# Performance work log

Hardware: AMD Instinct MI355X
Metric: run time of the kernel (lower is better)

Reference implementation:

```python
import jax, jax.numpy as jnp
import numpy as np

H = 64        # gru_hiddens
HEADS = 4     # n_heads
HID = 64      # n_hidden (is_concat=False -> out_features)
RT = 4        # role_types
APT = 3       # agents per type
N_AMB = 1023  # ambiguous agents; N = 1 + N_AMB = 1024
SLOPE = 0.2


def _leaky(x):
    return jnp.where(x >= 0, x, SLOPE * x)


def _linear(x, W, b):
    return x @ W.T + b


def setup_inputs() -> dict:
    key = jax.random.key(0)
    ks = jax.random.split(key, 18)
    s = 0.1
    return {
        "hidden": jax.random.normal(ks[0], (1, H), jnp.float32),
        "ambiguous": jax.random.normal(ks[1], (N_AMB, H), jnp.float32),
        "type_agents": jax.random.normal(ks[2], (RT, APT, 1, H), jnp.float32),
        # per-role-type routing MLPs and merge/self MLPs
        "W_self": jax.random.normal(ks[3], (H, H), jnp.float32) * s,
        "b_self": jnp.zeros((H,), jnp.float32),
        "W_merge": jax.random.normal(ks[4], (H, 2 * H), jnp.float32) * s,
        "b_merge": jnp.zeros((H,), jnp.float32),
        "W_trans": jax.random.normal(ks[5], (RT, H, H), jnp.float32) * s,
        "b_trans": jnp.zeros((RT, H), jnp.float32),
        # GATv2 params (no biases)
        "W_l": jax.random.normal(ks[6], (HEADS * HID, H), jnp.float32) * s,
        "W_r": jax.random.normal(ks[7], (HEADS * HID, H), jnp.float32) * s,
        "w_attn": jax.random.normal(ks[8], (HID,), jnp.float32) * s,
        # type_define MLP: 2H -> 64 -> 128 -> RT
        "Wd0": jax.random.normal(ks[9], (64, 2 * H), jnp.float32) * s,
        "bd0": jnp.zeros((64,), jnp.float32),
        "Wd1": jax.random.normal(ks[10], (128, 64), jnp.float32) * s,
        "bd1": jnp.zeros((128,), jnp.float32),
        "Wd2": jax.random.normal(ks[11], (RT, 128), jnp.float32) * s,
        "bd2": jnp.zeros((RT,), jnp.float32),
    }


def reference(hidden, ambiguous, type_agents,
              W_self, b_self, W_merge, b_merge, W_trans, b_trans,
              W_l, W_r, w_attn,
              Wd0, bd0, Wd1, bd1, Wd2, bd2):
    # per-role-type routing + merge
    hidden_1 = _linear(hidden, W_self, b_self)  # [1, H]
    for t in range(RT):
        # mean over agents of trans_mlp[t](agent)
        tmp = (jnp.einsum('aih,oh->aio', type_agents[t], W_trans[t]) + b_trans[t]).mean(axis=0)
        hidden_1 = _leaky(_linear(jnp.concatenate([hidden_1, tmp], axis=-1), W_merge, b_merge))

    h = jnp.concatenate([hidden_1, ambiguous], axis=0)  # [N, H], N = 1 + N_AMB
    n = h.shape[0]

    # GATv2 dense pairwise attention (adjacency all-True; dropout in eval = identity)
    g_l = (h @ W_l.T).reshape(n, HEADS, HID)
    g_r = (h @ W_r.T).reshape(n, HEADS, HID)
    # g_sum[i, j] = g_l[j] + g_r[i]  -> [N, N, HEADS, HID]
    g_sum = g_l[None, :, :, :] + g_r[:, None, :, :]
    e = jnp.einsum('ijhf,f->ijh', _leaky(g_sum), w_attn)  # [N, N, HEADS]
    a = jax.nn.softmax(e, axis=1)
    attn_res = jnp.einsum('ijh,jhf->ihf', a, g_r)  # [N, HEADS, HID]
    gat_out = attn_res.mean(axis=1)  # is_concat=False -> mean over heads, [N, HID]

    hidden_2 = gat_out[0]  # [HID]
    rep = jnp.broadcast_to(hidden_2[None, :], (ambiguous.shape[0], HID))
    x = jnp.concatenate([ambiguous, rep], axis=-1)  # [N_AMB, 2H]
    x = _leaky(_linear(x, Wd0, bd0))
    x = _leaky(_linear(x, Wd1, bd1))
    x = _linear(x, Wd2, bd2)
    return jax.nn.sigmoid(x)  # [N_AMB, RT]
```

## Files before the change

### kernel.cpp

```cpp
#include <hip/hip_runtime.h>
#include <math.h>

#define SLOPE 0.2f
#define KA_BLK 128
#define KA_ROWS 8
#define PART_STRIDE 320

__device__ __forceinline__ float leaky(float x) { return x >= 0.f ? x : SLOPE * x; }


__global__ __launch_bounds__(256) void kA_gat(
    const float* __restrict__ hidden, const float* __restrict__ ambiguous,
    const float* __restrict__ type_agents,
    const float* __restrict__ W_self, const float* __restrict__ b_self,
    const float* __restrict__ W_merge, const float* __restrict__ b_merge,
    const float* __restrict__ W_trans, const float* __restrict__ b_trans,
    const float* __restrict__ W_l, const float* __restrict__ W_r,
    const float* __restrict__ w_attn, float* __restrict__ ws)
{
    __shared__ __align__(16) float sh[128];
    __shared__ __align__(16) float tm[64];
    __shared__ __align__(16) float h1[64];
    __shared__ __align__(16) float hrow[KA_ROWS][64];

    const int t = threadIdx.x;
    const int o = t & 63;
    const int r = t >> 6;
    const int b = blockIdx.x;

    float4 wr[16];
    {
        const float4* Wr4 = (const float4*)(W_r + t * 64);
#pragma unroll
        for (int k = 0; k < 16; k++) wr[k] = Wr4[k];
    }

    if (r != 0) {
        int u = t - 64;
#pragma unroll
        for (int i = 0; i < 3; i++) {
            int idx = u + 192 * i;
            if (idx < KA_ROWS * 64) {
                int rl = idx >> 6, c = idx & 63;
                int j = b * KA_ROWS + rl;
                hrow[rl][c] = (j == 0) ? 0.f : ambiguous[(j - 1) * 64 + c];
            }
        }
    } else {
        float hv;
        {
            float acc = b_self[o];
            const float4* w4 = (const float4*)(W_self + o * 64);
#pragma unroll
            for (int k = 0; k < 16; k++) {
                float4 w = w4[k];
                acc += w.x * hidden[k*4+0] + w.y * hidden[k*4+1]
                     + w.z * hidden[k*4+2] + w.w * hidden[k*4+3];
            }
            hv = acc;
        }
        for (int tt = 0; tt < 4; tt++) {
            sh[o] = hv;
            tm[o] = (type_agents[tt*192 + o] + type_agents[tt*192 + 64 + o]
                   + type_agents[tt*192 + 128 + o]) * (1.f / 3.f);
            __threadfence_block();
            float tv = b_trans[tt*64 + o];
            {
                const float4* w4 = (const float4*)(W_trans + tt*4096 + o*64);
#pragma unroll
                for (int k = 0; k < 16; k++) {
                    float4 w = w4[k];
                    tv += w.x * tm[k*4+0] + w.y * tm[k*4+1]
                        + w.z * tm[k*4+2] + w.w * tm[k*4+3];
                }
            }
            sh[64 + o] = tv;
            __threadfence_block();
            float acc = b_merge[o];
            const float4* w4 = (const float4*)(W_merge + o * 128);
#pragma unroll
            for (int k = 0; k < 32; k++) {
                float4 w = w4[k];
                acc += w.x * sh[k*4+0] + w.y * sh[k*4+1]
                     + w.z * sh[k*4+2] + w.w * sh[k*4+3];
            }
            hv = leaky(acc);
            __threadfence_block();
        }
        h1[o] = hv;
    }
    __syncthreads();
    if (b == 0 && t < 64) hrow[0][o] = h1[o];

    float g0 = 0.f;
#pragma unroll
    for (int k = 0; k < 16; k++) {
        float4 w = wr[k];
        g0 += w.x * h1[k*4+0] + w.y * h1[k*4+1] + w.z * h1[k*4+2] + w.w * h1[k*4+3];
    }
    __syncthreads();

    float accl[KA_ROWS], accr[KA_ROWS];
#pragma unroll
    for (int rr = 0; rr < KA_ROWS; rr++) { accl[rr] = 0.f; accr[rr] = 0.f; }
    {
        const float4* Wl4 = (const float4*)(W_l + t * 64);
#pragma unroll
        for (int kk = 0; kk < 16; kk++) {
            float4 a = Wl4[kk];
            float4 c = wr[kk];
#pragma unroll
            for (int rr = 0; rr < KA_ROWS; rr++) {
                float x0 = hrow[rr][kk*4+0], x1 = hrow[rr][kk*4+1];
                float x2 = hrow[rr][kk*4+2], x3 = hrow[rr][kk*4+3];
                accl[rr] += a.x*x0 + a.y*x1 + a.z*x2 + a.w*x3;
                accr[rr] += c.x*x0 + c.y*x1 + c.z*x2 + c.w*x3;
            }
        }
    }

    const float wa = w_attn[o];
    float numsum = 0.f, denp = 0.f;
#pragma unroll
    for (int rr = 0; rr < KA_ROWS; rr++) {
        float ec = leaky(accl[rr] + g0) * wa;
#pragma unroll
        for (int off = 32; off; off >>= 1) ec += __shfl_xor(ec, off, 64);
        float w = expf(ec);
        numsum += w * accr[rr];
        denp   += w;
    }
    ws[b * PART_STRIDE + t] = numsum;
    if (o == 0) ws[b * PART_STRIDE + 256 + r] = denp;
}

__global__ __launch_bounds__(256) void kB_mlp(
    const float* __restrict__ ambiguous,
    const float* __restrict__ Wd0, const float* __restrict__ bd0,
    const float* __restrict__ Wd1, const float* __restrict__ bd1,
    const float* __restrict__ Wd2, const float* __restrict__ bd2,
    const float* __restrict__ ws, float* __restrict__ out)
{
    __shared__ __align__(16) float x[4][128];
    __shared__ __align__(16) float y0[4][64];
    __shared__ __align__(16) float y1[4][128];
    __shared__ __align__(16) float hs[4][64];
    const int t  = threadIdx.x;
    const int o  = t & 63;
    const int r  = t >> 6;
    const int r0 = blockIdx.x * 4;

    {
        int row = r0 + r;
        x[r][o] = (row < 1023) ? ambiguous[row * 64 + o] : 0.f;
    }

    float nsum = 0.f;
#pragma unroll 16
    for (int bb = 0; bb < KA_BLK; bb++) nsum += ws[bb * PART_STRIDE + t];

    float d = ws[o * PART_STRIDE + 256 + r]
            + ws[(o + 64) * PART_STRIDE + 256 + r];
#pragma unroll
    for (int off = 32; off; off >>= 1) d += __shfl_xor(d, off, 64);
    hs[r][o] = nsum / d;
    __syncthreads();
    if (t < 64) {
        float h2 = 0.25f * (hs[0][o] + hs[1][o] + hs[2][o] + hs[3][o]);
        x[0][64 + o] = h2; x[1][64 + o] = h2; x[2][64 + o] = h2; x[3][64 + o] = h2;
    }
    __syncthreads();

    {
        float acc = bd0[o];
        const float4* w4 = (const float4*)(Wd0 + o * 128);
        const float4* xr = (const float4*)(&x[r][0]);
#pragma unroll
        for (int kk = 0; kk < 32; kk++) {
            float4 w = w4[kk]; float4 xv = xr[kk];
            acc += w.x*xv.x + w.y*xv.y + w.z*xv.z + w.w*xv.w;
        }
        y0[r][o] = leaky(acc);
    }
    __syncthreads();

#pragma unroll
    for (int rep = 0; rep < 2; rep++) {
        int idx = rep * 256 + t;
        int rr = idx >> 7, oo = idx & 127;
        float acc = bd1[oo];
        const float4* w4 = (const float4*)(Wd1 + oo * 64);
        const float4* yr = (const float4*)(&y0[rr][0]);
#pragma unroll
        for (int kk = 0; kk < 16; kk++) {
            float4 w = w4[kk]; float4 yv = yr[kk];
            acc += w.x*yv.x + w.y*yv.y + w.z*yv.z + w.w*yv.w;
        }
        y1[rr][oo] = leaky(acc);
    }
    __syncthreads();

    if (t < 16) {
        int rr = t >> 2, c = t & 3;
        int row = r0 + rr;
        if (row < 1023) {
            float acc = bd2[c];
            const float4* w4 = (const float4*)(Wd2 + c * 128);
            const float4* yr = (const float4*)(&y1[rr][0]);
#pragma unroll
            for (int kk = 0; kk < 32; kk++) {
                float4 w = w4[kk]; float4 yv = yr[kk];
                acc += w.x*yv.x + w.y*yv.y + w.z*yv.z + w.w*yv.w;
            }
            out[row * 4 + c] = 1.f / (1.f + expf(-acc));
        }
    }
}

extern "C" void kernel_launch(void* const* d_in, const int* in_sizes, int n_in,
                              void* d_out, int out_size, void* d_ws, size_t ws_size,
                              hipStream_t stream)
{
    const float* hidden      = (const float*)d_in[0];
    const float* ambiguous   = (const float*)d_in[1];
    const float* type_agents = (const float*)d_in[2];
    const float* W_self      = (const float*)d_in[3];
    const float* b_self      = (const float*)d_in[4];
    const float* W_merge     = (const float*)d_in[5];
    const float* b_merge     = (const float*)d_in[6];
    const float* W_trans     = (const float*)d_in[7];
    const float* b_trans     = (const float*)d_in[8];
    const float* W_l         = (const float*)d_in[9];
    const float* W_r         = (const float*)d_in[10];
    const float* w_attn      = (const float*)d_in[11];
    const float* Wd0         = (const float*)d_in[12];
    const float* bd0         = (const float*)d_in[13];
    const float* Wd1         = (const float*)d_in[14];
    const float* bd1         = (const float*)d_in[15];
    const float* Wd2         = (const float*)d_in[16];
    const float* bd2         = (const float*)d_in[17];
    float* ws  = (float*)d_ws;
    float* out = (float*)d_out;

    kA_gat<<<KA_BLK, 256, 0, stream>>>(hidden, ambiguous, type_agents,
                                       W_self, b_self, W_merge, b_merge,
                                       W_trans, b_trans, W_l, W_r, w_attn, ws);
    kB_mlp<<<256, 256, 0, stream>>>(ambiguous, Wd0, bd0, Wd1, bd1, Wd2, bd2, ws, out);
}
```

Measured before the change: 129.1 us.

## Parallelize role-type transforms across warps and double GAT block count

The four per-role-type trans-MLP products are now computed in parallel by the four wavefronts before the serial merge chain, which shortens the critical path that only wavefront 0 ran before. W_l is preloaded into registers alongside W_r. The GAT kernel now launches 256 blocks of 4 rows instead of 128 blocks of 8, for more parallelism, and the MLP kernel sums twice as many partial sums and denominators. The cost is higher register pressure from holding both weight matrices and more redundant per-block work on the hidden-state chain.

```diff
diff --git a/kernel.cpp b/kernel.cpp
--- a/kernel.cpp
+++ b/kernel.cpp
@@ -2,8 +2,8 @@
 #include <math.h>
 
 #define SLOPE 0.2f
-#define KA_BLK 128
-#define KA_ROWS 8
+#define KA_BLK 256
+#define KA_ROWS 4
 #define PART_STRIDE 320
 
 __device__ __forceinline__ float leaky(float x) { return x >= 0.f ? x : SLOPE * x; }
@@ -18,8 +18,9 @@
     const float* __restrict__ W_l, const float* __restrict__ W_r,
     const float* __restrict__ w_attn, float* __restrict__ ws)
 {
-    __shared__ __align__(16) float sh[128];
-    __shared__ __align__(16) float tm[64];
+    __shared__ __align__(16) float tmean[4][64];
+    __shared__ __align__(16) float tmpv[4][64];
+    __shared__ __align__(16) float hstage[64];
     __shared__ __align__(16) float h1[64];
     __shared__ __align__(16) float hrow[KA_ROWS][64];
 
@@ -28,17 +29,46 @@
     const int r = t >> 6;
     const int b = blockIdx.x;
 
-    float4 wr[16];
+    float4 wr[16], wl[16];
     {
         const float4* Wr4 = (const float4*)(W_r + t * 64);
-#pragma unroll
-        for (int k = 0; k < 16; k++) wr[k] = Wr4[k];
+        const float4* Wl4 = (const float4*)(W_l + t * 64);
+#pragma unroll
+        for (int k = 0; k < 16; k++) { wr[k] = Wr4[k]; wl[k] = Wl4[k]; }
+    }
+
+    float hv = 0.f;
+    if (r == 0) {
+        float acc = b_self[o];
+        const float4* w4 = (const float4*)(W_self + o * 64);
+#pragma unroll
+        for (int k = 0; k < 16; k++) {
+            float4 w = w4[k];
+            acc += w.x * hidden[k*4+0] + w.y * hidden[k*4+1]
+                 + w.z * hidden[k*4+2] + w.w * hidden[k*4+3];
+        }
+        hv = acc;
+    }
+
+    tmean[r][o] = (type_agents[r*192 + o] + type_agents[r*192 + 64 + o]
+                 + type_agents[r*192 + 128 + o]) * (1.f / 3.f);
+    __threadfence_block();
+    {
+        float tv = b_trans[r*64 + o];
+        const float4* w4 = (const float4*)(W_trans + r*4096 + o*64);
+        const float4* tm4 = (const float4*)(&tmean[r][0]);
+#pragma unroll
+        for (int k = 0; k < 16; k++) {
+            float4 w = w4[k]; float4 m = tm4[k];
+            tv += w.x*m.x + w.y*m.y + w.z*m.z + w.w*m.w;
+        }
+        tmpv[r][o] = tv;
     }
 
     if (r != 0) {
         int u = t - 64;
 #pragma unroll
-        for (int i = 0; i < 3; i++) {
+        for (int i = 0; i < 2; i++) {
             int idx = u + 192 * i;
             if (idx < KA_ROWS * 64) {
                 int rl = idx >> 6, c = idx & 63;
@@ -46,43 +76,23 @@
                 hrow[rl][c] = (j == 0) ? 0.f : ambiguous[(j - 1) * 64 + c];
             }
         }
-    } else {
-        float hv;
-        {
-            float acc = b_self[o];
-            const float4* w4 = (const float4*)(W_self + o * 64);
-#pragma unroll
-            for (int k = 0; k < 16; k++) {
-                float4 w = w4[k];
-                acc += w.x * hidden[k*4+0] + w.y * hidden[k*4+1]
-                     + w.z * hidden[k*4+2] + w.w * hidden[k*4+3];
-            }
-            hv = acc;
-        }
+    }
+    __syncthreads();
+
+    if (r == 0) {
+        const float4* w4 = (const float4*)(W_merge + o * 128);
         for (int tt = 0; tt < 4; tt++) {
-            sh[o] = hv;
-            tm[o] = (type_agents[tt*192 + o] + type_agents[tt*192 + 64 + o]
-                   + type_agents[tt*192 + 128 + o]) * (1.f / 3.f);
-            __threadfence_block();
-            float tv = b_trans[tt*64 + o];
-            {
-                const float4* w4 = (const float4*)(W_trans + tt*4096 + o*64);
-#pragma unroll
-                for (int k = 0; k < 16; k++) {
-                    float4 w = w4[k];
-                    tv += w.x * tm[k*4+0] + w.y * tm[k*4+1]
-                        + w.z * tm[k*4+2] + w.w * tm[k*4+3];
-                }
-            }
-            sh[64 + o] = tv;
+            hstage[o] = hv;
             __threadfence_block();
             float acc = b_merge[o];
-            const float4* w4 = (const float4*)(W_merge + o * 128);
-#pragma unroll
-            for (int k = 0; k < 32; k++) {
-                float4 w = w4[k];
-                acc += w.x * sh[k*4+0] + w.y * sh[k*4+1]
-                     + w.z * sh[k*4+2] + w.w * sh[k*4+3];
+            const float4* hs4 = (const float4*)(&hstage[0]);
+            const float4* tp4 = (const float4*)(&tmpv[tt][0]);
+#pragma unroll
+            for (int k = 0; k < 16; k++) {
+                float4 w = w4[k];        float4 v = hs4[k];
+                acc += w.x*v.x + w.y*v.y + w.z*v.z + w.w*v.w;
+                float4 w2 = w4[16 + k];  float4 u = tp4[k];
+                acc += w2.x*u.x + w2.y*u.y + w2.z*u.z + w2.w*u.w;
             }
             hv = leaky(acc);
             __threadfence_block();
@@ -90,6 +100,7 @@
         h1[o] = hv;
     }
     __syncthreads();
+
     if (b == 0 && t < 64) hrow[0][o] = h1[o];
 
     float g0 = 0.f;
@@ -103,19 +114,16 @@
     float accl[KA_ROWS], accr[KA_ROWS];
 #pragma unroll
     for (int rr = 0; rr < KA_ROWS; rr++) { accl[rr] = 0.f; accr[rr] = 0.f; }
-    {
-        const float4* Wl4 = (const float4*)(W_l + t * 64);
-#pragma unroll
-        for (int kk = 0; kk < 16; kk++) {
-            float4 a = Wl4[kk];
-            float4 c = wr[kk];
-#pragma unroll
-            for (int rr = 0; rr < KA_ROWS; rr++) {
-                float x0 = hrow[rr][kk*4+0], x1 = hrow[rr][kk*4+1];
-                float x2 = hrow[rr][kk*4+2], x3 = hrow[rr][kk*4+3];
-                accl[rr] += a.x*x0 + a.y*x1 + a.z*x2 + a.w*x3;
-                accr[rr] += c.x*x0 + c.y*x1 + c.z*x2 + c.w*x3;
-            }
+#pragma unroll
+    for (int kk = 0; kk < 16; kk++) {
+        float4 a = wl[kk];
+        float4 c = wr[kk];
+#pragma unroll
+        for (int rr = 0; rr < KA_ROWS; rr++) {
+            float x0 = hrow[rr][kk*4+0], x1 = hrow[rr][kk*4+1];
+            float x2 = hrow[rr][kk*4+2], x3 = hrow[rr][kk*4+3];
+            accl[rr] += a.x*x0 + a.y*x1 + a.z*x2 + a.w*x3;
+            accr[rr] += c.x*x0 + c.y*x1 + c.z*x2 + c.w*x3;
         }
     }
 
@@ -160,7 +168,9 @@
     for (int bb = 0; bb < KA_BLK; bb++) nsum += ws[bb * PART_STRIDE + t];
 
     float d = ws[o * PART_STRIDE + 256 + r]
-            + ws[(o + 64) * PART_STRIDE + 256 + r];
+            + ws[(o + 64)  * PART_STRIDE + 256 + r]
+            + ws[(o + 128) * PART_STRIDE + 256 + r]
+            + ws[(o + 192) * PART_STRIDE + 256 + r];
 #pragma unroll
     for (int off = 32; off; off >>= 1) d += __shfl_xor(d, off, 64);
     hs[r][o] = nsum / d;
```

Result: faster. 123.9 us, median of 2 (-4.0%).
